# Performance work log

Hardware: AMD Instinct MI355X
Metric: run time of the kernel (lower is better)

The kernel has to match this reference:

```python
import jax, jax.numpy as jnp
import numpy as np

K = 3  # kernel size, padding=1, stride=1


def _patches(x):
    # x: [N,C,H,W] -> [N,C,9,H,W] of 3x3 neighborhoods (zero pad 1)
    N, C, H, W = x.shape
    xp = jnp.pad(x, ((0, 0), (0, 0), (1, 1), (1, 1)))
    return jnp.stack([xp[:, :, i:i + H, j:j + W] for i in range(K) for j in range(K)], axis=2)


def _conv25d(x, depth, fx, w0, w1, w2, b):
    # depth-banded 2.5D conv: 3 weight sets selected per (pixel, kernel-tap) by depth band
    N, C, H, W = x.shape
    O = w0.shape[0]
    px = _patches(x)                       # [N,C,9,H,W]
    d = _patches(depth)[:, 0]              # [N,9,H,W]
    center = d[:, K * K // 2:K * K // 2 + 1]  # [N,1,H,W]
    valid = ((d != 0) & (center != 0)).astype(x.dtype)
    d = d * valid
    center = d[:, K * K // 2:K * K // 2 + 1]
    gr = center / fx                       # grid_range, pixel_size = 1
    half = gr * 0.5
    m0 = (jnp.abs(d - (center + gr)) <= half).astype(x.dtype)  # behind plane
    m1 = (jnp.abs(d - center) < half).astype(x.dtype)          # on plane
    m2 = (jnp.abs(d - (center - gr)) <= half).astype(x.dtype)  # in front
    out = jnp.zeros((N, O, H, W), x.dtype)
    for w, m in ((w0, m0), (w1, m1), (w2, m2)):
        out = out + jnp.einsum('ock,nckhw->nohw', w.reshape(O, C, K * K), px * m[:, None])
    return out + b[None, :, None, None]


def _maxpool2(x):
    return jax.lax.reduce_window(x, -jnp.inf, jax.lax.max, (1, 1, 2, 2), (1, 1, 2, 2), 'VALID')


def setup_inputs() -> dict:
    key = jax.random.key(0)
    ks = jax.random.split(key, 16)
    N, H, W = 16, 224, 224

    def xavier(k, shape):
        if len(shape) == 4:
            rf = shape[2] * shape[3]
            fan_in, fan_out = shape[1] * rf, shape[0] * rf
        else:
            fan_out, fan_in = shape
        lim = float(np.sqrt(6.0 / (fan_in + fan_out)))
        return jax.random.uniform(k, shape, jnp.float32, -lim, lim)

    return {
        'x': jax.random.normal(ks[0], (N, 3, H, W), jnp.float32),
        'depth': jax.random.uniform(ks[1], (N, 1, H, W), jnp.float32, 1.0, 5.0),
        'fx': jnp.full((1,), 4.0, jnp.float32),
        'c1_w0': xavier(ks[2], (16, 3, 3, 3)),
        'c1_w1': xavier(ks[3], (16, 3, 3, 3)),
        'c1_w2': xavier(ks[4], (16, 3, 3, 3)),
        'c1_b': jnp.zeros((16,), jnp.float32),
        'c2_w0': xavier(ks[5], (16, 16, 3, 3)),
        'c2_w1': xavier(ks[6], (16, 16, 3, 3)),
        'c2_w2': xavier(ks[7], (16, 16, 3, 3)),
        'c2_b': jnp.zeros((16,), jnp.float32),
        'fc1_w': xavier(ks[8], (128, 16 * (W // 2) * (H // 2))),
        'fc1_b': jnp.zeros((128,), jnp.float32),
        'fc2_w': xavier(ks[9], (10, 128)),
        'fc2_b': jnp.zeros((10,), jnp.float32),
    }


def reference(x, depth, fx, c1_w0, c1_w1, c1_w2, c1_b, c2_w0, c2_w1, c2_w2, c2_b, fc1_w, fc1_b, fc2_w, fc2_b):
    h = jax.nn.relu(_conv25d(x, depth, fx, c1_w0, c1_w1, c1_w2, c1_b))
    h = _maxpool2(jax.nn.relu(_conv25d(h, depth, fx, c2_w0, c2_w1, c2_w2, c2_b)))
    h = h.reshape(h.shape[0], -1)          # [N, 16*112*112]
    h = h @ fc1_w.T + fc1_b                # no relu between fc1/fc2 (matches source)
    h = h @ fc2_w.T + fc2_b
    return jax.nn.log_softmax(h, axis=1)
```

## Files before the change

### kernel.cpp

```cpp
#include <hip/hip_runtime.h>
#include <hip/hip_fp16.h>
#include <stdint.h>

#define HH 224
#define HWD 224
#define HWP (HH*HWD)
#define PH 112
#define PW 112
#define PHW (PH*PW)
#define FCK 200704
#define KSEG 196

typedef _Float16 f16x8 __attribute__((ext_vector_type(8)));
typedef float f32x4 __attribute__((ext_vector_type(4)));

static __device__ __forceinline__ uint32_t pkh2(float a, float b) {
  __half2 h = __floats2half2_rn(a, b);
  return __builtin_bit_cast(uint32_t, h);
}
static __device__ __forceinline__ f32x4 mfma16(uint4 a, uint4 b, f32x4 c) {
  return __builtin_amdgcn_mfma_f32_16x16x32_f16(
      __builtin_bit_cast(f16x8, a), __builtin_bit_cast(f16x8, b), c, 0, 0, 0);
}


__global__ __launch_bounds__(256, 4) void conv1_kernel(
    const float* __restrict__ x, const float* __restrict__ depth,
    const float* __restrict__ fxp,
    const float* __restrict__ w0, const float* __restrict__ w1,
    const float* __restrict__ w2, const float* __restrict__ bias,
    uint32_t* __restrict__ sel, __half* __restrict__ h1t) {
  __shared__ __align__(16) __half ts[324*24];
  __shared__ __align__(16) uint4 wlds[15*64];
  __shared__ float dt[324];
  __shared__ uint32_t sbits[256];
  __shared__ __align__(16) __half hbuf[1024];
  int tid = threadIdx.x;
  int lane = tid & 63, wid = tid >> 6;
  int r = lane & 15;
  int tapPar = lane >> 5;
  int c0 = ((lane >> 4) & 1) * 8;
  float bo = bias[r];
  float fx = fxp[0];

  #pragma unroll
  for (int it = 0; it < 4; ++it) {
    int t = tid + it*256;
    int tc = min(t, 959);
    int ln = tc & 63; int pj = tc >> 6;
    int p = pj / 3, j = pj % 3;
    int o = ln & 15; int tap = p*2 + (ln >> 5);
    int cbase = ((ln >> 4) & 1) * 8;
    const float* wj = (j == 0) ? w0 : (j == 1) ? w1 : w2;
    float f[8];
    #pragma unroll
    for (int e = 0; e < 8; ++e) {
      int c = cbase + e;
      float v = wj[o*27 + min(c,2)*9 + min(tap,8)];
      f[e] = (tap <= 8 && c < 3) ? v : 0.f;
    }
    if (t < 960) {
      uint4 wv = { pkh2(f[0],f[1]), pkh2(f[2],f[3]), pkh2(f[4],f[5]), pkh2(f[6],f[7]) };
      wlds[pj*64 + ln] = wv;
    }
  }

  int tbase = blockIdx.x * 4;
  float pf[2][3]; float pd[2];
  {
    int tile = tbase;
    int n = tile/196, rem = tile%196, br = rem/14, bc = rem%14;
    int y0 = br*16 - 1, x0 = bc*16 - 1;
    const float* xn = x + (size_t)n*3*HWP;
    const float* dn = depth + (size_t)n*HWP;
    #pragma unroll
    for (int it = 0; it < 2; ++it) {
      int p = min(tid + it*256, 323);
      int yy = y0 + p/18, xx = x0 + p%18;
      int gy = min(max(yy,0),HH-1), gx = min(max(xx,0),HWD-1);
      size_t off = (size_t)gy*HWD + gx;
      pf[it][0] = xn[off]; pf[it][1] = xn[HWP+off]; pf[it][2] = xn[2*HWP+off];
      float dv = dn[off];
      pd[it] = (yy>=0 && yy<HH && xx>=0 && xx<HWD) ? dv : 0.f;
    }
  }

  for (int ti = 0; ti < 4; ++ti) {
    int tile = tbase + ti;
    int n = tile/196, rem = tile%196, br = rem/14, bc = rem%14;
    #pragma unroll
    for (int it = 0; it < 2; ++it) {
      int p = tid + it*256;
      if (p < 324) {
        uint4 v0 = { pkh2(pf[it][0], pf[it][1]), pkh2(pf[it][2], 0.f), 0u, 0u };
        uint4 z  = { 0u, 0u, 0u, 0u };
        *(uint4*)(ts + p*24)      = v0;
        *(uint4*)(ts + p*24 + 8)  = z;
        *(uint4*)(ts + p*24 + 16) = z;
        dt[p] = pd[it];
      }
    }
    if (ti < 3) {
      int tile2 = tile + 1;
      int n2 = tile2/196, rem2 = tile2%196, br2 = rem2/14, bc2 = rem2%14;
      int y0 = br2*16 - 1, x0 = bc2*16 - 1;
      const float* xn = x + (size_t)n2*3*HWP;
      const float* dn = depth + (size_t)n2*HWP;
      #pragma unroll
      for (int it = 0; it < 2; ++it) {
        int p = min(tid + it*256, 323);
        int yy = y0 + p/18, xx = x0 + p%18;
        int gy = min(max(yy,0),HH-1), gx = min(max(xx,0),HWD-1);
        size_t off = (size_t)gy*HWD + gx;
        pf[it][0] = xn[off]; pf[it][1] = xn[HWP+off]; pf[it][2] = xn[2*HWP+off];
        float dv = dn[off];
        pd[it] = (yy>=0 && yy<HH && xx>=0 && xx<HWD) ? dv : 0.f;
      }
    }
    __syncthreads();
    {
      int py = tid >> 4, px = tid & 15;
      float c = dt[(py+1)*18 + (px+1)];
      float gr = c / fx;
      float hf = gr * 0.5f;
      uint32_t bits = 0;
      #pragma unroll
      for (int i = 0; i < 3; ++i)
        #pragma unroll
        for (int j = 0; j < 3; ++j) {
          float d = dt[(py+i)*18 + (px+j)];
          int k = i*3 + j;
          uint32_t bb = 0;
          if (fabsf(d - (c + gr)) <= hf) bb |= 1u;
          if (fabsf(d - c) < hf)         bb |= 2u;
          if (fabsf(d - (c - gr)) <= hf) bb |= 4u;
          bits |= bb << (3*k);
        }
      sbits[tid] = bits;
      sel[(size_t)n*HWP + (br*16 + py)*HWD + bc*16 + px] = bits;
    }
    __syncthreads();
    uint32_t svc[4];
    #pragma unroll
    for (int ty = 0; ty < 4; ++ty) svc[ty] = sbits[(wid*4 + ty)*16 + r];
    f32x4 acc[4] = {{0,0,0,0},{0,0,0,0},{0,0,0,0},{0,0,0,0}};
    #pragma unroll
    for (int p = 0; p < 5; ++p) {
      int ta = 2*p, tb = (2*p+1 > 8) ? 8 : 2*p+1;
      int dyL = tapPar ? tb/3 : ta/3;
      int dxL = tapPar ? tb%3 : ta%3;
      int shL = 3*(tapPar ? 2*p+1 : 2*p);
      uint4 a[4];
      #pragma unroll
      for (int ty = 0; ty < 4; ++ty) {
        int ly = wid*4 + ty;
        a[ty] = *(const uint4*)(ts + ((ly + dyL)*18 + (r + dxL))*24 + c0);
      }
      #pragma unroll
      for (int j = 0; j < 3; ++j) {
        uint4 bf = wlds[(p*3 + j)*64 + lane];
        #pragma unroll
        for (int ty = 0; ty < 4; ++ty) {
          uint32_t msk = 0u - ((svc[ty] >> (shL + j)) & 1u);
          uint4 am = { a[ty].x & msk, a[ty].y & msk, a[ty].z & msk, a[ty].w & msk };
          acc[ty] = mfma16(am, bf, acc[ty]);
        }
      }
    }
    #pragma unroll
    for (int ty = 0; ty < 4; ++ty) {
      int gy = br*16 + wid*4 + ty;
      #pragma unroll
      for (int e = 0; e < 4; ++e) {
        float v = fmaxf(acc[ty][e] + bo, 0.f);
        hbuf[wid*256 + ((lane>>4)*4 + e)*16 + r] = __float2half(v);
      }
      uint2 hw = *(uint2*)&hbuf[wid*256 + lane*4];
      *(uint2*)(h1t + ((size_t)(n*HWP + gy*HWD) + bc*16)*16 + lane*4) = hw;
    }
    __syncthreads();
  }
}

__global__ __launch_bounds__(256, 4) void conv2_kernel(
    const __half* __restrict__ h1t, const uint32_t* __restrict__ sel,
    const float* __restrict__ w0, const float* __restrict__ w1,
    const float* __restrict__ w2, const float* __restrict__ bias,
    __half* __restrict__ pooled) {
  __shared__ __align__(16) __half ts[324*24];
  __shared__ __align__(16) uint4 wlds[15*64];
  __shared__ float pl[64*17];
  int tid = threadIdx.x;
  int lane = tid & 63, wid = tid >> 6;
  int r = lane & 15;
  int tapPar = lane >> 5;
  int c0 = ((lane >> 4) & 1) * 8;
  float bo = bias[r];

  #pragma unroll
  for (int it = 0; it < 4; ++it) {
    int t = tid + it*256;
    int tc = min(t, 959);
    int ln = tc & 63; int pj = tc >> 6;
    int p = pj / 3, j = pj % 3;
    int o = ln & 15; int tap = p*2 + (ln >> 5);
    int cbase = ((ln >> 4) & 1) * 8;
    const float* wj = (j == 0) ? w0 : (j == 1) ? w1 : w2;
    const float* wp = wj + o*144 + cbase*9 + tap;
    float f[8];
    #pragma unroll
    for (int e = 0; e < 8; ++e) {
      float v = wp[e*9];
      f[e] = (tap <= 8) ? v : 0.f;
    }
    if (t < 960) {
      uint4 wv = { pkh2(f[0],f[1]), pkh2(f[2],f[3]), pkh2(f[4],f[5]), pkh2(f[6],f[7]) };
      wlds[pj*64 + ln] = wv;
    }
  }

  int tbase = blockIdx.x * 4;
  uint4 st[3]; uint32_t sv[4];
  {
    int tile = tbase;
    int n = tile/196, rem = tile%196, br = rem/14, bc = rem%14;
    int y0 = br*16 - 1, x0 = bc*16 - 1;
    const __half* hn = h1t + (size_t)n*HWP*16;
    #pragma unroll
    for (int it = 0; it < 3; ++it) {
      int w = min(tid + it*256, 647);
      int p = w >> 1, hh = w & 1;
      int gy = min(max(y0 + p/18, 0), HH-1);
      int gx = min(max(x0 + p%18, 0), HWD-1);
      st[it] = *(const uint4*)(hn + ((size_t)(gy*HWD + gx))*16 + hh*8);
    }
    #pragma unroll
    for (int ty = 0; ty < 4; ++ty)
      sv[ty] = sel[(size_t)n*HWP + (br*16 + wid*4 + ty)*HWD + bc*16 + r];
  }

  for (int ti = 0; ti < 4; ++ti) {
    int tile = tbase + ti;
    int n = tile/196, rem = tile%196, br = rem/14, bc = rem%14;
    #pragma unroll
    for (int it = 0; it < 3; ++it) {
      int w = tid + it*256;
      if (w < 648) {
        int p = w >> 1, hh = w & 1;
        *(uint4*)(ts + p*24 + hh*8) = st[it];
      }
    }
    uint32_t svc[4];
    #pragma unroll
    for (int ty = 0; ty < 4; ++ty) svc[ty] = sv[ty];
    if (ti < 3) {
      int tile2 = tile + 1;
      int n2 = tile2/196, rem2 = tile2%196, br2 = rem2/14, bc2 = rem2%14;
      int y0 = br2*16 - 1, x0 = bc2*16 - 1;
      const __half* hn = h1t + (size_t)n2*HWP*16;
      #pragma unroll
      for (int it = 0; it < 3; ++it) {
        int w = min(tid + it*256, 647);
        int p = w >> 1, hh = w & 1;
        int gy = min(max(y0 + p/18, 0), HH-1);
        int gx = min(max(x0 + p%18, 0), HWD-1);
        st[it] = *(const uint4*)(hn + ((size_t)(gy*HWD + gx))*16 + hh*8);
      }
      #pragma unroll
      for (int ty = 0; ty < 4; ++ty)
        sv[ty] = sel[(size_t)n2*HWP + (br2*16 + wid*4 + ty)*HWD + bc2*16 + r];
    }
    __syncthreads();
    f32x4 acc[4] = {{0,0,0,0},{0,0,0,0},{0,0,0,0},{0,0,0,0}};
    #pragma unroll
    for (int p = 0; p < 5; ++p) {
      int ta = 2*p, tb = (2*p+1 > 8) ? 8 : 2*p+1;
      int dyL = tapPar ? tb/3 : ta/3;
      int dxL = tapPar ? tb%3 : ta%3;
      int shL = 3*(tapPar ? 2*p+1 : 2*p);
      uint4 a[4];
      #pragma unroll
      for (int ty = 0; ty < 4; ++ty) {
        int ly = wid*4 + ty;
        a[ty] = *(const uint4*)(ts + ((ly + dyL)*18 + (r + dxL))*24 + c0);
      }
      #pragma unroll
      for (int j = 0; j < 3; ++j) {
        uint4 bf = wlds[(p*3 + j)*64 + lane];
        #pragma unroll
        for (int ty = 0; ty < 4; ++ty) {
          uint32_t msk = 0u - ((svc[ty] >> (shL + j)) & 1u);
          uint4 am = { a[ty].x & msk, a[ty].y & msk, a[ty].z & msk, a[ty].w & msk };
          acc[ty] = mfma16(am, bf, acc[ty]);
        }
      }
    }
    #pragma unroll
    for (int yp = 0; yp < 2; ++yp) {
      f32x4 v0 = acc[yp*2], v1 = acc[yp*2+1];
      float m00 = fmaxf(fmaxf(v0[0]+bo, 0.f), fmaxf(v0[1]+bo, 0.f));
      float m01 = fmaxf(fmaxf(v0[2]+bo, 0.f), fmaxf(v0[3]+bo, 0.f));
      float m10 = fmaxf(fmaxf(v1[0]+bo, 0.f), fmaxf(v1[1]+bo, 0.f));
      float m11 = fmaxf(fmaxf(v1[2]+bo, 0.f), fmaxf(v1[3]+bo, 0.f));
      int prow = wid*2 + yp;
      int pc0 = (lane >> 4)*2;
      pl[(prow*8 + pc0)*17 + r]     = fmaxf(m00, m10);
      pl[(prow*8 + pc0 + 1)*17 + r] = fmaxf(m01, m11);
    }
    __syncthreads();
    for (int t = tid; t < 1024; t += 256) {
      int oo = t >> 6; int pix = t & 63;
      int pr = pix >> 3, pc = pix & 7;
      pooled[(size_t)(n*16 + oo)*PHW + (br*8 + pr)*PW + bc*8 + pc] =
          __float2half(pl[pix*17 + oo]);
    }
    __syncthreads();
  }
}

__global__ __launch_bounds__(256) void fc1_kernel(
    const __half* __restrict__ hin, const float* __restrict__ wgt,
    float* __restrict__ partial) {
  __shared__ __align__(16) uint4 alds[2][256];
  __shared__ __align__(16) uint4 wlds[2][2][256];
  __shared__ __align__(16) f32x4 cacc[2][256];
  int tid = threadIdx.x;
  int b = blockIdx.x;
  int snum = (b & 7)*98 + (b >> 3);
  int kseg = snum >> 2;
  int grp  = snum & 3;
  int obase = grp * 32;
  int lane = tid & 63, wid = tid >> 6;
  int q8 = tid & 15, row = tid >> 4;
  int sslot = (q8>>2)*64 + (row | ((q8&3) << 4));
  const __half* hp0 = hin + (size_t)row*FCK + kseg*1024 + q8*8;
  const float* wq0  = wgt + (size_t)(obase + row)*FCK + kseg*1024 + q8*8;
  const float* wq1  = wgt + (size_t)(obase + 16 + row)*FCK + kseg*1024 + q8*8;
  uint4 hv; float4 w0a, w0b, w1a, w1b;
  hv  = *(const uint4*)hp0;
  w0a = *(const float4*)wq0; w0b = *(const float4*)(wq0 + 4);
  w1a = *(const float4*)wq1; w1b = *(const float4*)(wq1 + 4);
  f32x4 acc0 = {0,0,0,0}, acc1 = {0,0,0,0};
  for (int ch = 0; ch < 8; ++ch) {
    int buf = ch & 1;
    alds[buf][sslot] = hv;
    wlds[buf][0][sslot] = (uint4){ pkh2(w0a.x,w0a.y), pkh2(w0a.z,w0a.w),
                                   pkh2(w0b.x,w0b.y), pkh2(w0b.z,w0b.w) };
    wlds[buf][1][sslot] = (uint4){ pkh2(w1a.x,w1a.y), pkh2(w1a.z,w1a.w),
                                   pkh2(w1b.x,w1b.y), pkh2(w1b.z,w1b.w) };
    if (ch < 7) {
      hv  = *(const uint4*)(hp0 + (ch+1)*128);
      w0a = *(const float4*)(wq0 + (ch+1)*128); w0b = *(const float4*)(wq0 + (ch+1)*128 + 4);
      w1a = *(const float4*)(wq1 + (ch+1)*128); w1b = *(const float4*)(wq1 + (ch+1)*128 + 4);
    }
    __syncthreads();
    uint4 av = alds[buf][wid*64 + lane];
    acc0 = mfma16(av, wlds[buf][0][wid*64 + lane], acc0);
    acc1 = mfma16(av, wlds[buf][1][wid*64 + lane], acc1);
  }
  cacc[0][wid*64 + lane] = acc0;
  cacc[1][wid*64 + lane] = acc1;
  __syncthreads();
  {
    int l = tid & 63, e = tid >> 6;
    int nn = (l >> 4)*4 + e;
    int oo = l & 15;
    #pragma unroll
    for (int g = 0; g < 2; ++g) {
      float s = cacc[g][l][e] + cacc[g][64 + l][e] + cacc[g][128 + l][e] + cacc[g][192 + l][e];
      partial[((size_t)kseg*16 + nn)*128 + obase + g*16 + oo] = s;
    }
  }
}

__global__ __launch_bounds__(256) void fc2_kernel(
    const float* __restrict__ partial, const float* __restrict__ fc1b,
    const float* __restrict__ w, const float* __restrict__ b,
    float* __restrict__ out) {
  __shared__ float psum[256];
  __shared__ float row[128];
  __shared__ float v[10];
  __shared__ float lse;
  int n = blockIdx.x, t = threadIdx.x;
  {
    int o = t & 127, half = t >> 7;
    const float* pp = partial + ((size_t)(half*98)*16 + n)*128 + o;
    float s = 0.f;
    for (int k = 0; k < 98; ++k) s += pp[(size_t)k*2048];
    psum[t] = s;
  }
  __syncthreads();
  if (t < 128) row[t] = fc1b[t] + psum[t] + psum[t + 128];
  __syncthreads();
  {
    int wv = t >> 6, lane = t & 63;
    for (int d = wv; d < 10; d += 4) {
      float acc = w[d*128 + lane]*row[lane] + w[d*128 + 64 + lane]*row[64 + lane];
      acc += __shfl_xor(acc, 1);  acc += __shfl_xor(acc, 2);
      acc += __shfl_xor(acc, 4);  acc += __shfl_xor(acc, 8);
      acc += __shfl_xor(acc, 16); acc += __shfl_xor(acc, 32);
      if (lane == 0) v[d] = acc + b[d];
    }
  }
  __syncthreads();
  if (t == 0) {
    float m = v[0];
    for (int i = 1; i < 10; ++i) m = fmaxf(m, v[i]);
    float se = 0.f;
    for (int i = 0; i < 10; ++i) se += expf(v[i] - m);
    lse = m + logf(se);
  }
  __syncthreads();
  if (t < 10) out[n*10 + t] = v[t] - lse;
}

extern "C" void kernel_launch(void* const* d_in, const int* in_sizes, int n_in,
                              void* d_out, int out_size, void* d_ws, size_t ws_size,
                              hipStream_t stream) {
  const float* x     = (const float*)d_in[0];
  const float* depth = (const float*)d_in[1];
  const float* fx    = (const float*)d_in[2];
  const float* c1w0  = (const float*)d_in[3];
  const float* c1w1  = (const float*)d_in[4];
  const float* c1w2  = (const float*)d_in[5];
  const float* c1b   = (const float*)d_in[6];
  const float* c2w0  = (const float*)d_in[7];
  const float* c2w1  = (const float*)d_in[8];
  const float* c2w2  = (const float*)d_in[9];
  const float* c2b   = (const float*)d_in[10];
  const float* fc1w  = (const float*)d_in[11];
  const float* fc1b  = (const float*)d_in[12];
  const float* fc2w  = (const float*)d_in[13];
  const float* fc2b  = (const float*)d_in[14];
  float* out = (float*)d_out;

  char* ws = (char*)d_ws;
  uint32_t* sel  = (uint32_t*)ws;
  __half* h1t    = (__half*)(ws + 3211264);
  __half* pooled = (__half*)(ws + 28901376);
  float* partial = (float*)(ws + 35323904);

  conv1_kernel<<<784, 256, 0, stream>>>(x, depth, fx, c1w0, c1w1, c1w2, c1b, sel, h1t);
  conv2_kernel<<<784, 256, 0, stream>>>(h1t, sel, c2w0, c2w1, c2w2, c2b, pooled);
  fc1_kernel<<<784, 256, 0, stream>>>(pooled, fc1w, partial);
  fc2_kernel<<<16, 256, 0, stream>>>(partial, fc1b, fc2w, fc2b, out);
}
```

Before: 99.92 us.

## Load conv2 and fc1 MFMA operands directly from global memory, dropping LDS staging

In conv2, the register-prefetched LDS halo tile is removed. Each lane now reads its 3x3-neighborhood input fragments straight from global memory with clamped coordinates, and the per-tile select words are loaded without prefetch. In fc1, the double-buffered LDS staging of activations and weights is replaced by per-wave direct global loads in MFMA fragment layout, removing the per-chunk barriers. The aim is to cut LDS traffic and synchronisation, at the cost of redundant global/L2 reads (conv2 halo reuse is lost) and less latency hiding from the removed prefetch.

```diff
diff --git a/kernel.cpp b/kernel.cpp
--- a/kernel.cpp
+++ b/kernel.cpp
@@ -187,7 +187,6 @@
     const float* __restrict__ w0, const float* __restrict__ w1,
     const float* __restrict__ w2, const float* __restrict__ bias,
     __half* __restrict__ pooled) {
-  __shared__ __align__(16) __half ts[324*24];
   __shared__ __align__(16) uint4 wlds[15*64];
   __shared__ float pl[64*17];
   int tid = threadIdx.x;
@@ -218,59 +217,17 @@
       wlds[pj*64 + ln] = wv;
     }
   }
+  __syncthreads();
 
   int tbase = blockIdx.x * 4;
-  uint4 st[3]; uint32_t sv[4];
-  {
-    int tile = tbase;
-    int n = tile/196, rem = tile%196, br = rem/14, bc = rem%14;
-    int y0 = br*16 - 1, x0 = bc*16 - 1;
-    const __half* hn = h1t + (size_t)n*HWP*16;
-    #pragma unroll
-    for (int it = 0; it < 3; ++it) {
-      int w = min(tid + it*256, 647);
-      int p = w >> 1, hh = w & 1;
-      int gy = min(max(y0 + p/18, 0), HH-1);
-      int gx = min(max(x0 + p%18, 0), HWD-1);
-      st[it] = *(const uint4*)(hn + ((size_t)(gy*HWD + gx))*16 + hh*8);
-    }
-    #pragma unroll
-    for (int ty = 0; ty < 4; ++ty)
-      sv[ty] = sel[(size_t)n*HWP + (br*16 + wid*4 + ty)*HWD + bc*16 + r];
-  }
-
   for (int ti = 0; ti < 4; ++ti) {
     int tile = tbase + ti;
     int n = tile/196, rem = tile%196, br = rem/14, bc = rem%14;
-    #pragma unroll
-    for (int it = 0; it < 3; ++it) {
-      int w = tid + it*256;
-      if (w < 648) {
-        int p = w >> 1, hh = w & 1;
-        *(uint4*)(ts + p*24 + hh*8) = st[it];
-      }
-    }
+    const __half* hn = h1t + (size_t)n*HWP*16;
     uint32_t svc[4];
     #pragma unroll
-    for (int ty = 0; ty < 4; ++ty) svc[ty] = sv[ty];
-    if (ti < 3) {
-      int tile2 = tile + 1;
-      int n2 = tile2/196, rem2 = tile2%196, br2 = rem2/14, bc2 = rem2%14;
-      int y0 = br2*16 - 1, x0 = bc2*16 - 1;
-      const __half* hn = h1t + (size_t)n2*HWP*16;
-      #pragma unroll
-      for (int it = 0; it < 3; ++it) {
-        int w = min(tid + it*256, 647);
-        int p = w >> 1, hh = w & 1;
-        int gy = min(max(y0 + p/18, 0), HH-1);
-        int gx = min(max(x0 + p%18, 0), HWD-1);
-        st[it] = *(const uint4*)(hn + ((size_t)(gy*HWD + gx))*16 + hh*8);
-      }
-      #pragma unroll
-      for (int ty = 0; ty < 4; ++ty)
-        sv[ty] = sel[(size_t)n2*HWP + (br2*16 + wid*4 + ty)*HWD + bc2*16 + r];
-    }
-    __syncthreads();
+    for (int ty = 0; ty < 4; ++ty)
+      svc[ty] = sel[(size_t)n*HWP + (br*16 + wid*4 + ty)*HWD + bc*16 + r];
     f32x4 acc[4] = {{0,0,0,0},{0,0,0,0},{0,0,0,0},{0,0,0,0}};
     #pragma unroll
     for (int p = 0; p < 5; ++p) {
@@ -278,11 +235,12 @@
       int dyL = tapPar ? tb/3 : ta/3;
       int dxL = tapPar ? tb%3 : ta%3;
       int shL = 3*(tapPar ? 2*p+1 : 2*p);
+      int gx = min(max(bc*16 + r + dxL - 1, 0), HWD-1);
       uint4 a[4];
       #pragma unroll
       for (int ty = 0; ty < 4; ++ty) {
-        int ly = wid*4 + ty;
-        a[ty] = *(const uint4*)(ts + ((ly + dyL)*18 + (r + dxL))*24 + c0);
+        int gy = min(max(br*16 + wid*4 + ty + dyL - 1, 0), HH-1);
+        a[ty] = *(const uint4*)(hn + ((size_t)(gy*HWD + gx))*16 + c0);
       }
       #pragma unroll
       for (int j = 0; j < 3; ++j) {
@@ -321,8 +279,6 @@
 __global__ __launch_bounds__(256) void fc1_kernel(
     const __half* __restrict__ hin, const float* __restrict__ wgt,
     float* __restrict__ partial) {
-  __shared__ __align__(16) uint4 alds[2][256];
-  __shared__ __align__(16) uint4 wlds[2][2][256];
   __shared__ __align__(16) f32x4 cacc[2][256];
   int tid = threadIdx.x;
   int b = blockIdx.x;
@@ -331,32 +287,24 @@
   int grp  = snum & 3;
   int obase = grp * 32;
   int lane = tid & 63, wid = tid >> 6;
-  int q8 = tid & 15, row = tid >> 4;
-  int sslot = (q8>>2)*64 + (row | ((q8&3) << 4));
-  const __half* hp0 = hin + (size_t)row*FCK + kseg*1024 + q8*8;
-  const float* wq0  = wgt + (size_t)(obase + row)*FCK + kseg*1024 + q8*8;
-  const float* wq1  = wgt + (size_t)(obase + 16 + row)*FCK + kseg*1024 + q8*8;
-  uint4 hv; float4 w0a, w0b, w1a, w1b;
-  hv  = *(const uint4*)hp0;
-  w0a = *(const float4*)wq0; w0b = *(const float4*)(wq0 + 4);
-  w1a = *(const float4*)wq1; w1b = *(const float4*)(wq1 + 4);
+  int row = lane & 15;
+  int koct = lane >> 4;
+  size_t kb = (size_t)kseg*1024 + wid*256 + koct*8;
+  const __half* ap  = hin + (size_t)row*FCK + kb;
+  const float*  wp0 = wgt + (size_t)(obase + row)*FCK + kb;
+  const float*  wp1 = wp0 + (size_t)16*FCK;
   f32x4 acc0 = {0,0,0,0}, acc1 = {0,0,0,0};
-  for (int ch = 0; ch < 8; ++ch) {
-    int buf = ch & 1;
-    alds[buf][sslot] = hv;
-    wlds[buf][0][sslot] = (uint4){ pkh2(w0a.x,w0a.y), pkh2(w0a.z,w0a.w),
-                                   pkh2(w0b.x,w0b.y), pkh2(w0b.z,w0b.w) };
-    wlds[buf][1][sslot] = (uint4){ pkh2(w1a.x,w1a.y), pkh2(w1a.z,w1a.w),
-                                   pkh2(w1b.x,w1b.y), pkh2(w1b.z,w1b.w) };
-    if (ch < 7) {
-      hv  = *(const uint4*)(hp0 + (ch+1)*128);
-      w0a = *(const float4*)(wq0 + (ch+1)*128); w0b = *(const float4*)(wq0 + (ch+1)*128 + 4);
-      w1a = *(const float4*)(wq1 + (ch+1)*128); w1b = *(const float4*)(wq1 + (ch+1)*128 + 4);
-    }
-    __syncthreads();
-    uint4 av = alds[buf][wid*64 + lane];
-    acc0 = mfma16(av, wlds[buf][0][wid*64 + lane], acc0);
-    acc1 = mfma16(av, wlds[buf][1][wid*64 + lane], acc1);
+  #pragma unroll
+  for (int s = 0; s < 8; ++s) {
+    uint4 av = *(const uint4*)(ap + s*32);
+    float4 wa = *(const float4*)(wp0 + s*32);
+    float4 wb = *(const float4*)(wp0 + s*32 + 4);
+    float4 wc = *(const float4*)(wp1 + s*32);
+    float4 wd = *(const float4*)(wp1 + s*32 + 4);
+    uint4 bf0 = { pkh2(wa.x,wa.y), pkh2(wa.z,wa.w), pkh2(wb.x,wb.y), pkh2(wb.z,wb.w) };
+    uint4 bf1 = { pkh2(wc.x,wc.y), pkh2(wc.z,wc.w), pkh2(wd.x,wd.y), pkh2(wd.z,wd.w) };
+    acc0 = mfma16(av, bf0, acc0);
+    acc1 = mfma16(av, bf1, acc1);
   }
   cacc[0][wid*64 + lane] = acc0;
   cacc[1][wid*64 + lane] = acc1;
```

New measurement: 100.9 us. About the same (+1.0%).
